# Optimization experiments

Hardware: AMD Instinct MI355X
Metric: run time of the kernel (lower is better)

## Reference

```python
import jax, jax.numpy as jnp
import numpy as np

N = 50000
E = 600000
D_IN, D_HID, D_OUT = 128, 128, 64


def gcn_conv(x, edge_index, W, b):
    """PyG GCNConv: add self-loops, symmetric deg^{-1/2} normalization,
    linear transform, scatter-add aggregation, bias."""
    n = x.shape[0]
    loop = jnp.arange(n, dtype=edge_index.dtype)
    src = jnp.concatenate([edge_index[0], loop])
    dst = jnp.concatenate([edge_index[1], loop])
    h = x @ W  # [N, out]
    deg = jax.ops.segment_sum(jnp.ones_like(dst, dtype=h.dtype), dst, num_segments=n)
    dinv = jnp.where(deg > 0, jax.lax.rsqrt(jnp.maximum(deg, 1e-12)), 0.0)
    norm = dinv[src] * dinv[dst]  # [E+N]
    msg = h[src] * norm[:, None]  # gather + scale
    out = jax.ops.segment_sum(msg, dst, num_segments=n)  # scatter-add
    return out + b


def setup_inputs() -> dict:
    key = jax.random.key(0)
    k1, k2, k3, k4 = jax.random.split(key, 4)
    x = jax.random.normal(k1, (N, D_IN), dtype=jnp.float32)
    edge_index = jax.random.randint(k2, (2, E), 0, N, dtype=jnp.int64)
    s1 = (1.0 / np.sqrt(D_IN)).astype(np.float32) if False else np.float32(1.0 / np.sqrt(D_IN))
    s2 = np.float32(1.0 / np.sqrt(D_HID))
    W1 = jax.random.normal(k3, (D_IN, D_HID), dtype=jnp.float32) * s1
    b1 = jnp.zeros((D_HID,), dtype=jnp.float32)
    W2 = jax.random.normal(k4, (D_HID, D_OUT), dtype=jnp.float32) * s2
    b2 = jnp.zeros((D_OUT,), dtype=jnp.float32)
    return {"x": x, "edge_index": edge_index, "W1": W1, "b1": b1, "W2": W2, "b2": b2}


def reference(x, edge_index, W1, b1, W2, b2):
    # eval mode: dropout p = 0
    h = jax.nn.relu(gcn_conv(x, edge_index, W1, b1))
    return gcn_conv(h, edge_index, W2, b2)
```

## Files before the change

kernel.cpp:

```cpp
#include <hip/hip_runtime.h>
#include <hip/hip_bf16.h>
#include <stdint.h>

#define DIN 128
#define DHID 128
#define DOUT2 64

__device__ __forceinline__ unsigned short f2bf(float f) {
    unsigned u = __float_as_uint(f);
    u += 0x7fffu + ((u >> 16) & 1u);
    return (unsigned short)(u >> 16);
}
__device__ __forceinline__ float bf2f(unsigned short b) {
    return __uint_as_float(((unsigned)b) << 16);
}

__global__ void detect_i64_kernel(const unsigned* ei, int* flag) {
    int t = threadIdx.x;
    unsigned hi = ei[2 * t + 1];
    unsigned long long vote = __ballot(hi == 0u);
    if (t == 0) *flag = (vote == ~0ull) ? 1 : 0;
}

__global__ void deg_count_kernel(const int* ei32, const long long* ei64, const int* flag,
                                 unsigned* deg, int E) {
    int e = blockIdx.x * blockDim.x + threadIdx.x;
    if (e >= E) return;
    int mode = *flag;
    int d = mode ? (int)ei64[(size_t)E + e] : ei32[(size_t)E + e];
    atomicAdd(&deg[d], 1u);
}

__global__ void dinv_kernel(const unsigned* deg, float* dinv, int N) {
    int i = blockIdx.x * blockDim.x + threadIdx.x;
    if (i < N) dinv[i] = 1.0f / sqrtf((float)(deg[i] + 1u));
}

__global__ __launch_bounds__(256) void scan_blocksum_kernel(const unsigned* deg, int* bsum,
                                                            int N) {
    __shared__ int s[256];
    int t = threadIdx.x;
    int base = blockIdx.x * 1024 + t * 4;
    int sum = 0;
    if (base + 3 < N) {
        int4 v = *(const int4*)((const int*)deg + base);
        sum = v.x + v.y + v.z + v.w;
    } else {
        for (int j = 0; j < 4; j++)
            if (base + j < N) sum += (int)deg[base + j];
    }
    s[t] = sum;
    __syncthreads();
    for (int off = 128; off > 0; off >>= 1) {
        if (t < off) s[t] += s[t + off];
        __syncthreads();
    }
    if (t == 0) bsum[blockIdx.x] = s[0];
}

__global__ __launch_bounds__(256) void scan_bsum_kernel(int* bsum, int* row_ptr, int nb, int N) {
    __shared__ int s[256];
    int t = threadIdx.x;
    int v = (t < nb) ? bsum[t] : 0;
    s[t] = v;
    __syncthreads();
    for (int off = 1; off < 256; off <<= 1) {
        int u = (t >= off) ? s[t - off] : 0;
        __syncthreads();
        s[t] += u;
        __syncthreads();
    }
    if (t < nb) bsum[t] = s[t] - v;
    if (t == 255) row_ptr[N] = s[255];
}

__global__ __launch_bounds__(256) void scan_write_kernel(const unsigned* deg, const int* bsum,
                                                         int* row_ptr, int* cursor, int N) {
    __shared__ int s[256];
    int t = threadIdx.x;
    int base = blockIdx.x * 1024 + t * 4;
    int d[4];
    int sum = 0;
#pragma unroll
    for (int j = 0; j < 4; j++) {
        int idx = base + j;
        d[j] = (idx < N) ? (int)deg[idx] : 0;
        sum += d[j];
    }
    s[t] = sum;
    __syncthreads();
    for (int off = 1; off < 256; off <<= 1) {
        int u = (t >= off) ? s[t - off] : 0;
        __syncthreads();
        s[t] += u;
        __syncthreads();
    }
    int run = bsum[blockIdx.x] + s[t] - sum;
#pragma unroll
    for (int j = 0; j < 4; j++) {
        int idx = base + j;
        if (idx < N) {
            row_ptr[idx] = run;
            cursor[idx] = run;
            run += d[j];
        }
    }
}

__global__ void scatter_kernel(const int* ei32, const long long* ei64, const int* flag,
                               const float* dinv, int* cursor, int* csr_src, float* csr_w,
                               int E) {
    int e = blockIdx.x * blockDim.x + threadIdx.x;
    if (e >= E) return;
    int mode = *flag;
    int s, d;
    if (mode) {
        s = (int)ei64[e];
        d = (int)ei64[(size_t)E + e];
    } else {
        s = ei32[e];
        d = ei32[(size_t)E + e];
    }
    int pos = atomicAdd(&cursor[d], 1);
    csr_src[pos] = s;
    csr_w[pos] = dinv[s];
}

template <int DO>
__global__ __launch_bounds__(256, 2) void gemm_kernel(const float* __restrict__ A,
                                                      const float* __restrict__ W,
                                                      unsigned short* __restrict__ out, int M) {
    constexpr int CG  = DO / 4;
    constexpr int TYN = 256 / CG;
    constexpr int RM  = 64 / TYN;
    __shared__ float As[64 * 64];
    __shared__ float Bs[64 * DO];
    const int tid = threadIdx.x;
    const int row0 = blockIdx.x * 64;
    const int tx = tid % CG, ty = tid / CG;

    float acc[RM][4];
#pragma unroll
    for (int r = 0; r < RM; r++) acc[r][0] = acc[r][1] = acc[r][2] = acc[r][3] = 0.f;

    for (int k0 = 0; k0 < 128; k0 += 64) {
        for (int idx = tid; idx < 64 * 16; idx += 256) {
            int r = idx >> 4, cc = idx & 15;
            int row = row0 + r;
            float4 v = make_float4(0.f, 0.f, 0.f, 0.f);
            if (row < M) v = ((const float4*)A)[(size_t)row * 32 + (k0 >> 2) + cc];
            ((float4*)As)[idx] = v;
        }
        for (int idx = tid; idx < 64 * CG; idx += 256) {
            int r = idx / CG, cc = idx % CG;
            ((float4*)Bs)[idx] = ((const float4*)W)[(size_t)(k0 + r) * CG + cc];
        }
        __syncthreads();
#pragma unroll 8
        for (int k = 0; k < 64; k++) {
            float4 b = ((const float4*)Bs)[k * CG + tx];
#pragma unroll
            for (int r = 0; r < RM; r++) {
                float a = As[(ty * RM + r) * 64 + k];
                acc[r][0] = fmaf(a, b.x, acc[r][0]);
                acc[r][1] = fmaf(a, b.y, acc[r][1]);
                acc[r][2] = fmaf(a, b.z, acc[r][2]);
                acc[r][3] = fmaf(a, b.w, acc[r][3]);
            }
        }
        __syncthreads();
    }
#pragma unroll
    for (int r = 0; r < RM; r++) {
        int row = row0 + ty * RM + r;
        if (row < M) {
            ushort4 v;
            v.x = f2bf(acc[r][0]);
            v.y = f2bf(acc[r][1]);
            v.z = f2bf(acc[r][2]);
            v.w = f2bf(acc[r][3]);
            ((ushort4*)out)[(size_t)row * CG + tx] = v;
        }
    }
}

template <int D, bool RELU>
__global__ __launch_bounds__(128) void agg_kernel(const unsigned short* __restrict__ h,
                                                  const int* __restrict__ csr_src,
                                                  const float* __restrict__ csr_w,
                                                  const int* __restrict__ row_ptr,
                                                  const float* __restrict__ dinv,
                                                  const float* __restrict__ bias,
                                                  float* __restrict__ out, int N) {
    constexpr int CHUNK = 128;
    __shared__ int s_src[CHUNK];
    __shared__ float s_w[CHUNK];
    const int i = blockIdx.x;
    const int c = threadIdx.x;
    const float di = dinv[i];
    float acc = di * bf2f(h[(size_t)i * D + c]);
    const int start = row_ptr[i], end = row_ptr[i + 1];
    for (int base = start; base < end; base += CHUNK) {
        int m = min(CHUNK, end - base);
        for (int j = c; j < m; j += D) {
            s_src[j] = csr_src[base + j];
            s_w[j] = csr_w[base + j];
        }
        __syncthreads();
        for (int j = 0; j < m; j++) {
            acc = fmaf(s_w[j], bf2f(h[(size_t)s_src[j] * D + c]), acc);
        }
        __syncthreads();
    }
    float r = di * acc + bias[c];
    out[(size_t)i * D + c] = RELU ? fmaxf(r, 0.f) : r;
}

extern "C" void kernel_launch(void* const* d_in, const int* in_sizes, int n_in,
                              void* d_out, int out_size, void* d_ws, size_t ws_size,
                              hipStream_t stream) {
    const float* x  = (const float*)d_in[0];
    const void*  ei = d_in[1];
    const float* W1 = (const float*)d_in[2];
    const float* b1 = (const float*)d_in[3];
    const float* W2 = (const float*)d_in[4];
    const float* b2 = (const float*)d_in[5];
    float* out = (float*)d_out;

    const int N = in_sizes[0] / DIN;
    const int E = in_sizes[1] / 2;

    char* ws = (char*)d_ws;
    size_t off = 0;
    auto alloc = [&](size_t bytes) -> void* {
        void* p = ws + off;
        off += (bytes + 255) & ~(size_t)255;
        return p;
    };
    unsigned*       deg  = (unsigned*)alloc((size_t)N * 4);
    float*          dinv = (float*)alloc((size_t)N * 4);
    int*            rowp = (int*)alloc((size_t)(N + 1) * 4);
    int*            curs = (int*)alloc((size_t)N * 4);
    int*            flag = (int*)alloc(256);
    int*            bsum = (int*)alloc(1024 * 4);
    int*            csrs = (int*)alloc((size_t)E * 4);
    float*          csrw = (float*)alloc((size_t)E * 4);
    unsigned short* h1   = (unsigned short*)alloc((size_t)N * DHID * 2);
    float*          o1   = (float*)alloc((size_t)N * DHID * 4);
    unsigned short* h2   = h1;

    const int nb = (N + 1023) / 1024;

    hipMemsetAsync(deg, 0, (size_t)N * 4, stream);
    detect_i64_kernel<<<1, 64, 0, stream>>>((const unsigned*)ei, flag);
    deg_count_kernel<<<(E + 255) / 256, 256, 0, stream>>>((const int*)ei, (const long long*)ei,
                                                          flag, deg, E);
    dinv_kernel<<<(N + 255) / 256, 256, 0, stream>>>(deg, dinv, N);
    scan_blocksum_kernel<<<nb, 256, 0, stream>>>(deg, bsum, N);
    scan_bsum_kernel<<<1, 256, 0, stream>>>(bsum, rowp, nb, N);
    scan_write_kernel<<<nb, 256, 0, stream>>>(deg, bsum, rowp, curs, N);
    scatter_kernel<<<(E + 255) / 256, 256, 0, stream>>>((const int*)ei, (const long long*)ei,
                                                        flag, dinv, curs, csrs, csrw, E);
    gemm_kernel<DHID><<<(N + 63) / 64, 256, 0, stream>>>(x, W1, h1, N);
    agg_kernel<DHID, true><<<N, DHID, 0, stream>>>(h1, csrs, csrw, rowp, dinv, b1, o1, N);
    gemm_kernel<DOUT2><<<(N + 63) / 64, 256, 0, stream>>>(o1, W2, h2, N);
    agg_kernel<DOUT2, false><<<N, DOUT2, 0, stream>>>(h2, csrs, csrw, rowp, dinv, b2, out, N);
}
```

Baseline: 269.2 us.

## Use wave-per-node aggregation with packed bf16 loads and bf16 hidden activations

Aggregation now assigns one 64-lane wavefront per destination node, with four nodes per 256-thread block, instead of one block per node. Each lane reads neighbor indices and weights straight from the CSR arrays, so the shared-memory staging and block barriers are gone. In layer 1 each lane loads two bf16 values packed into a 32-bit word, and the gather loop is unrolled by four into two accumulators. The hidden activations between layers are stored as bf16 rather than fp32, which halves that write and the second GEMM's read, at some cost in precision.

```diff
diff --git a/kernel.cpp b/kernel.cpp
--- a/kernel.cpp
+++ b/kernel.cpp
@@ -14,6 +14,8 @@
 __device__ __forceinline__ float bf2f(unsigned short b) {
     return __uint_as_float(((unsigned)b) << 16);
 }
+__device__ __forceinline__ float bflo(unsigned v) { return __uint_as_float(v << 16); }
+__device__ __forceinline__ float bfhi(unsigned v) { return __uint_as_float(v & 0xffff0000u); }
 
 __global__ void detect_i64_kernel(const unsigned* ei, int* flag) {
     int t = threadIdx.x;
@@ -126,8 +128,8 @@
     csr_w[pos] = dinv[s];
 }
 
-template <int DO>
-__global__ __launch_bounds__(256, 2) void gemm_kernel(const float* __restrict__ A,
+template <int DO, typename AT>
+__global__ __launch_bounds__(256, 2) void gemm_kernel(const AT* __restrict__ A,
                                                       const float* __restrict__ W,
                                                       unsigned short* __restrict__ out, int M) {
     constexpr int CG  = DO / 4;
@@ -148,7 +150,14 @@
             int r = idx >> 4, cc = idx & 15;
             int row = row0 + r;
             float4 v = make_float4(0.f, 0.f, 0.f, 0.f);
-            if (row < M) v = ((const float4*)A)[(size_t)row * 32 + (k0 >> 2) + cc];
+            if (row < M) {
+                if constexpr (sizeof(AT) == 4) {
+                    v = ((const float4*)A)[(size_t)row * 32 + (k0 >> 2) + cc];
+                } else {
+                    ushort4 u = ((const ushort4*)A)[(size_t)row * 32 + (k0 >> 2) + cc];
+                    v = make_float4(bf2f(u.x), bf2f(u.y), bf2f(u.z), bf2f(u.w));
+                }
+            }
             ((float4*)As)[idx] = v;
         }
         for (int idx = tid; idx < 64 * CG; idx += 256) {
@@ -184,36 +193,90 @@
     }
 }
 
-template <int D, bool RELU>
-__global__ __launch_bounds__(128) void agg_kernel(const unsigned short* __restrict__ h,
+template <int D, bool RELU, typename OT>
+__global__ __launch_bounds__(256) void agg_kernel(const unsigned short* __restrict__ h,
                                                   const int* __restrict__ csr_src,
                                                   const float* __restrict__ csr_w,
                                                   const int* __restrict__ row_ptr,
                                                   const float* __restrict__ dinv,
                                                   const float* __restrict__ bias,
-                                                  float* __restrict__ out, int N) {
-    constexpr int CHUNK = 128;
-    __shared__ int s_src[CHUNK];
-    __shared__ float s_w[CHUNK];
-    const int i = blockIdx.x;
-    const int c = threadIdx.x;
+                                                  OT* __restrict__ out, int N) {
+    const int wid = threadIdx.x >> 6;
+    const int lane = threadIdx.x & 63;
+    const int i = blockIdx.x * 4 + wid;
+    if (i >= N) return;
     const float di = dinv[i];
-    float acc = di * bf2f(h[(size_t)i * D + c]);
     const int start = row_ptr[i], end = row_ptr[i + 1];
-    for (int base = start; base < end; base += CHUNK) {
-        int m = min(CHUNK, end - base);
-        for (int j = c; j < m; j += D) {
-            s_src[j] = csr_src[base + j];
-            s_w[j] = csr_w[base + j];
-        }
-        __syncthreads();
-        for (int j = 0; j < m; j++) {
-            acc = fmaf(s_w[j], bf2f(h[(size_t)s_src[j] * D + c]), acc);
-        }
-        __syncthreads();
-    }
-    float r = di * acc + bias[c];
-    out[(size_t)i * D + c] = RELU ? fmaxf(r, 0.f) : r;
+
+    if constexpr (D == 128) {
+        const unsigned* hu = (const unsigned*)h;
+        unsigned sv = hu[(size_t)i * 64 + lane];
+        float a0 = di * bflo(sv), b0 = di * bfhi(sv);
+        float a1 = 0.f, b1 = 0.f;
+        int j = start;
+        for (; j + 4 <= end; j += 4) {
+            int s0 = csr_src[j], s1 = csr_src[j + 1], s2 = csr_src[j + 2], s3 = csr_src[j + 3];
+            float w0 = csr_w[j], w1 = csr_w[j + 1], w2 = csr_w[j + 2], w3 = csr_w[j + 3];
+            unsigned v0 = hu[(size_t)s0 * 64 + lane];
+            unsigned v1 = hu[(size_t)s1 * 64 + lane];
+            unsigned v2 = hu[(size_t)s2 * 64 + lane];
+            unsigned v3 = hu[(size_t)s3 * 64 + lane];
+            a0 = fmaf(w0, bflo(v0), a0);
+            b0 = fmaf(w0, bfhi(v0), b0);
+            a1 = fmaf(w1, bflo(v1), a1);
+            b1 = fmaf(w1, bfhi(v1), b1);
+            a0 = fmaf(w2, bflo(v2), a0);
+            b0 = fmaf(w2, bfhi(v2), b0);
+            a1 = fmaf(w3, bflo(v3), a1);
+            b1 = fmaf(w3, bfhi(v3), b1);
+        }
+        for (; j < end; ++j) {
+            int s0 = csr_src[j];
+            float w0 = csr_w[j];
+            unsigned v0 = hu[(size_t)s0 * 64 + lane];
+            a0 = fmaf(w0, bflo(v0), a0);
+            b0 = fmaf(w0, bfhi(v0), b0);
+        }
+        float rx = di * (a0 + a1) + bias[2 * lane];
+        float ry = di * (b0 + b1) + bias[2 * lane + 1];
+        if (RELU) {
+            rx = fmaxf(rx, 0.f);
+            ry = fmaxf(ry, 0.f);
+        }
+        if constexpr (sizeof(OT) == 2) {
+            unsigned pv = (unsigned)f2bf(rx) | ((unsigned)f2bf(ry) << 16);
+            ((unsigned*)out)[(size_t)i * 64 + lane] = pv;
+        } else {
+            float2 pv = make_float2(rx, ry);
+            ((float2*)out)[(size_t)i * 64 + lane] = pv;
+        }
+    } else {
+        float a0 = di * bf2f(h[(size_t)i * 64 + lane]);
+        float a1 = 0.f;
+        int j = start;
+        for (; j + 4 <= end; j += 4) {
+            int s0 = csr_src[j], s1 = csr_src[j + 1], s2 = csr_src[j + 2], s3 = csr_src[j + 3];
+            float w0 = csr_w[j], w1 = csr_w[j + 1], w2 = csr_w[j + 2], w3 = csr_w[j + 3];
+            float v0 = bf2f(h[(size_t)s0 * 64 + lane]);
+            float v1 = bf2f(h[(size_t)s1 * 64 + lane]);
+            float v2 = bf2f(h[(size_t)s2 * 64 + lane]);
+            float v3 = bf2f(h[(size_t)s3 * 64 + lane]);
+            a0 = fmaf(w0, v0, a0);
+            a1 = fmaf(w1, v1, a1);
+            a0 = fmaf(w2, v2, a0);
+            a1 = fmaf(w3, v3, a1);
+        }
+        for (; j < end; ++j) {
+            a0 = fmaf(csr_w[j], bf2f(h[(size_t)csr_src[j] * 64 + lane]), a0);
+        }
+        float r = di * (a0 + a1) + bias[lane];
+        if (RELU) r = fmaxf(r, 0.f);
+        if constexpr (sizeof(OT) == 2) {
+            out[(size_t)i * 64 + lane] = (OT)f2bf(r);
+        } else {
+            out[(size_t)i * 64 + lane] = r;
+        }
+    }
 }
 
 extern "C" void kernel_launch(void* const* d_in, const int* in_sizes, int n_in,
@@ -246,7 +309,7 @@
     int*            csrs = (int*)alloc((size_t)E * 4);
     float*          csrw = (float*)alloc((size_t)E * 4);
     unsigned short* h1   = (unsigned short*)alloc((size_t)N * DHID * 2);
-    float*          o1   = (float*)alloc((size_t)N * DHID * 4);
+    unsigned short* o1   = (unsigned short*)alloc((size_t)N * DHID * 2);
     unsigned short* h2   = h1;
 
     const int nb = (N + 1023) / 1024;
@@ -261,8 +324,10 @@
     scan_write_kernel<<<nb, 256, 0, stream>>>(deg, bsum, rowp, curs, N);
     scatter_kernel<<<(E + 255) / 256, 256, 0, stream>>>((const int*)ei, (const long long*)ei,
                                                         flag, dinv, curs, csrs, csrw, E);
-    gemm_kernel<DHID><<<(N + 63) / 64, 256, 0, stream>>>(x, W1, h1, N);
-    agg_kernel<DHID, true><<<N, DHID, 0, stream>>>(h1, csrs, csrw, rowp, dinv, b1, o1, N);
-    gemm_kernel<DOUT2><<<(N + 63) / 64, 256, 0, stream>>>(o1, W2, h2, N);
-    agg_kernel<DOUT2, false><<<N, DOUT2, 0, stream>>>(h2, csrs, csrw, rowp, dinv, b2, out, N);
-}
+    gemm_kernel<DHID, float><<<(N + 63) / 64, 256, 0, stream>>>(x, W1, h1, N);
+    agg_kernel<DHID, true, unsigned short><<<(N + 3) / 4, 256, 0, stream>>>(h1, csrs, csrw, rowp,
+                                                                            dinv, b1, o1, N);
+    gemm_kernel<DOUT2, unsigned short><<<(N + 63) / 64, 256, 0, stream>>>(o1, W2, h2, N);
+    agg_kernel<DOUT2, false, float><<<(N + 3) / 4, 256, 0, stream>>>(h2, csrs, csrw, rowp, dinv,
+                                                                     b2, out, N);
+}
```

Result: slower. 274.6 us (+2.0%).
